# Kernel optimization log

Measured on AMD Instinct MI355X. Metric: run time of the kernel, lower is better.

## Reference

```python
import jax, jax.numpy as jnp
import numpy as np

D_MODEL = 1024
NHEAD = 16
HEAD_DIM = D_MODEL // NHEAD


def setup_inputs() -> dict:
    key = jax.random.key(0)
    ks = jax.random.split(key, 11)
    B, S = 4, 2048
    s = 1.0 / np.sqrt(D_MODEL)
    return {
        "q": jax.random.normal(ks[0], (B, S, D_MODEL), jnp.float32),
        "k": jax.random.normal(ks[1], (B, S, D_MODEL), jnp.float32),
        "v": jax.random.normal(ks[2], (B, S, D_MODEL), jnp.float32),
        "Wq": jax.random.normal(ks[3], (D_MODEL, D_MODEL), jnp.float32) * s,
        "bq": jnp.zeros((D_MODEL,), jnp.float32),
        "Wk": jax.random.normal(ks[4], (D_MODEL, D_MODEL), jnp.float32) * s,
        "bk": jnp.zeros((D_MODEL,), jnp.float32),
        "Wv": jax.random.normal(ks[5], (D_MODEL, D_MODEL), jnp.float32) * s,
        "bv": jnp.zeros((D_MODEL,), jnp.float32),
        "Wo": jax.random.normal(ks[6], (D_MODEL, D_MODEL), jnp.float32) * s,
        "bo": jnp.zeros((D_MODEL,), jnp.float32),
    }


def reference(q, k, v, Wq, bq, Wk, bk, Wv, bv, Wo, bo):
    B, S, _ = q.shape
    H, Dh = NHEAD, HEAD_DIM

    def proj(x, W, b):  # nn.Linear: x @ W.T + b, then split heads -> [B,H,S,Dh]
        y = x @ W.T + b
        return y.reshape(B, S, H, Dh).transpose(0, 2, 1, 3)

    qh = proj(q, Wq, bq)
    kh = proj(k, Wk, bk)
    vh = proj(v, Wv, bv)

    scores = jnp.einsum("bhsd,bhtd->bhst", qh, kh) / jnp.sqrt(jnp.float32(Dh))
    attn = jax.nn.softmax(scores, axis=-1)
    out = jnp.einsum("bhst,bhtd->bhsd", attn, vh)  # [B,H,S,Dh]
    out = out.transpose(0, 2, 1, 3).reshape(B, S, H * Dh)
    return out @ Wo.T + bo
```

## Files before the change

kernel.cpp:

```cpp
#include <hip/hip_runtime.h>


typedef short bf16x8 __attribute__((ext_vector_type(8)));
typedef short bf16x4 __attribute__((ext_vector_type(4)));
typedef float f32x4 __attribute__((ext_vector_type(4)));

__device__ __forceinline__ short f2bf(float x) {
    union { float f; unsigned int u; } un; un.f = x;
    unsigned int u = un.u;
    return (short)(unsigned short)((u + 0x7fffu + ((u >> 16) & 1u)) >> 16);
}

__global__ __launch_bounds__(256) void cvt_bf16(const float* __restrict__ s,
                                                unsigned short* __restrict__ d, int n4) {
    int i = blockIdx.x * blockDim.x + threadIdx.x;
    int stride = gridDim.x * blockDim.x;
    const float4* s4 = reinterpret_cast<const float4*>(s);
    bf16x4* d4 = reinterpret_cast<bf16x4*>(d);
    for (; i < n4; i += stride) {
        float4 x = s4[i];
        bf16x4 y;
        y[0] = f2bf(x.x); y[1] = f2bf(x.y); y[2] = f2bf(x.z); y[3] = f2bf(x.w);
        d4[i] = y;
    }
}

__device__ __forceinline__ void gll16(const void* g, void* l) {
    __builtin_amdgcn_global_load_lds(
        (const __attribute__((address_space(1))) void*)g,
        (__attribute__((address_space(3))) void*)l, 16, 0, 0);
}

template <int MODE>
__global__ __launch_bounds__(256) void gemm_bt(const unsigned short* __restrict__ A,
                                               const unsigned short* __restrict__ Bw,
                                               const float* __restrict__ bias,
                                               float scale,
                                               void* __restrict__ Cout) {
    __shared__ unsigned short As[128 * 32];
    __shared__ unsigned short Bs[128 * 32];
    const int tid = threadIdx.x;
    const int m0 = blockIdx.y * 128, n0 = blockIdx.x * 128;
    const int wave = tid >> 6, lane = tid & 63;
    const int wm = (wave >> 1) * 64, wn = (wave & 1) * 64;
    const int l15 = lane & 15, quad = lane >> 4;
    const int sr = tid >> 2;
    const int sc = (tid & 3) * 8;

    f32x4 acc[4][4] = {};

    for (int k0 = 0; k0 < 1024; k0 += 32) {
        __syncthreads();
#pragma unroll
        for (int ro = 0; ro < 2; ++ro) {
            gll16(&A[(size_t)(m0 + ro * 64 + sr) * 1024 + k0 + sc], &As[ro * 2048 + tid * 8]);
            gll16(&Bw[(size_t)(n0 + ro * 64 + sr) * 1024 + k0 + sc], &Bs[ro * 2048 + tid * 8]);
        }
        __syncthreads();
        bf16x8 a[4], b[4];
#pragma unroll
        for (int i = 0; i < 4; ++i)
            a[i] = *reinterpret_cast<bf16x8*>(&As[(wm + i * 16 + l15) * 32 + quad * 8]);
#pragma unroll
        for (int j = 0; j < 4; ++j)
            b[j] = *reinterpret_cast<bf16x8*>(&Bs[(wn + j * 16 + l15) * 32 + quad * 8]);
#pragma unroll
        for (int i = 0; i < 4; ++i)
#pragma unroll
            for (int j = 0; j < 4; ++j)
                acc[i][j] = __builtin_amdgcn_mfma_f32_16x16x32_bf16(a[i], b[j], acc[i][j], 0, 0, 0);
    }

#pragma unroll
    for (int i = 0; i < 4; ++i) {
#pragma unroll
        for (int j = 0; j < 4; ++j) {
#pragma unroll
            for (int r = 0; r < 4; ++r) {
                int m = m0 + wm + i * 16 + quad * 4 + r;
                int n = n0 + wn + j * 16 + l15;
                float val = (acc[i][j][r] + bias[n]) * scale;
                if (MODE == 0) {
                    reinterpret_cast<float*>(Cout)[(size_t)m * 1024 + n] = val;
                } else {
                    int b_ = m >> 11, s = m & 2047, h = n >> 6, d = n & 63;
                    size_t off = (MODE == 1)
                                     ? ((size_t)((b_ * 16 + h) * 2048 + s) * 64 + d)
                                     : ((size_t)((b_ * 16 + h) * 64 + d) * 2048 + s);
                    reinterpret_cast<unsigned short*>(Cout)[off] = (unsigned short)f2bf(val);
                }
            }
        }
    }
}

__global__ __launch_bounds__(256) void flash_attn(const unsigned short* __restrict__ Qh,
                                                  const unsigned short* __restrict__ Kh,
                                                  const unsigned short* __restrict__ Vt,
                                                  unsigned short* __restrict__ Oa) {
    constexpr int LD = 72;
    __shared__ unsigned short Ks[64 * LD];
    __shared__ unsigned short Vs[64 * LD];
    __shared__ unsigned short Ps[128 * LD];
    const int tid = threadIdx.x;
    const int bh = blockIdx.y;
    const int q0 = blockIdx.x * 128;
    const unsigned short* Qb = Qh + (size_t)bh * 2048 * 64;
    const unsigned short* Kb = Kh + (size_t)bh * 2048 * 64;
    const unsigned short* Vb = Vt + (size_t)bh * 64 * 2048;
    const int wave = tid >> 6, lane = tid & 63;
    const int l15 = lane & 15, quad = lane >> 4;
    const int wq = wave * 32;

    bf16x8 qreg[2][2];
#pragma unroll
    for (int i = 0; i < 2; ++i)
#pragma unroll
        for (int kk = 0; kk < 2; ++kk)
            qreg[i][kk] = *reinterpret_cast<const bf16x8*>(
                &Qb[(size_t)(q0 + wq + i * 16 + l15) * 64 + kk * 32 + quad * 8]);

    f32x4 o[2][4] = {};
    float lpart[2] = {0.f, 0.f};
    const int sr = tid >> 3;
    const int sc = (tid & 7) * 8;

    for (int kv0 = 0; kv0 < 2048; kv0 += 64) {
        __syncthreads();
#pragma unroll
        for (int ro = 0; ro < 2; ++ro) {
            int r = ro * 32 + sr;
            *reinterpret_cast<bf16x8*>(&Ks[r * LD + sc]) =
                *reinterpret_cast<const bf16x8*>(&Kb[(size_t)(kv0 + r) * 64 + sc]);
            *reinterpret_cast<bf16x8*>(&Vs[r * LD + sc]) =
                *reinterpret_cast<const bf16x8*>(&Vb[(size_t)r * 2048 + kv0 + sc]);
        }
        __syncthreads();

        f32x4 sacc[2][4] = {};
#pragma unroll
        for (int kk = 0; kk < 2; ++kk) {
            bf16x8 ak[4];
#pragma unroll
            for (int j = 0; j < 4; ++j)
                ak[j] = *reinterpret_cast<bf16x8*>(&Ks[(j * 16 + l15) * LD + kk * 32 + quad * 8]);
#pragma unroll
            for (int i = 0; i < 2; ++i)
#pragma unroll
                for (int j = 0; j < 4; ++j)
                    sacc[i][j] = __builtin_amdgcn_mfma_f32_16x16x32_bf16(ak[j], qreg[i][kk], sacc[i][j], 0, 0, 0);
        }

#pragma unroll
        for (int i = 0; i < 2; ++i) {
#pragma unroll
            for (int j = 0; j < 4; ++j) {
                float p0 = __expf(sacc[i][j][0]);
                float p1 = __expf(sacc[i][j][1]);
                float p2 = __expf(sacc[i][j][2]);
                float p3 = __expf(sacc[i][j][3]);
                lpart[i] += (p0 + p1) + (p2 + p3);
                bf16x4 pk;
                pk[0] = f2bf(p0); pk[1] = f2bf(p1); pk[2] = f2bf(p2); pk[3] = f2bf(p3);
                *reinterpret_cast<bf16x4*>(&Ps[(wq + i * 16 + l15) * LD + j * 16 + quad * 4]) = pk;
            }
        }

#pragma unroll
        for (int kk = 0; kk < 2; ++kk) {
            bf16x8 ap[2];
#pragma unroll
            for (int i = 0; i < 2; ++i)
                ap[i] = *reinterpret_cast<bf16x8*>(&Ps[(wq + i * 16 + l15) * LD + kk * 32 + quad * 8]);
#pragma unroll
            for (int n = 0; n < 4; ++n) {
                bf16x8 bv = *reinterpret_cast<bf16x8*>(&Vs[(n * 16 + l15) * LD + kk * 32 + quad * 8]);
#pragma unroll
                for (int i = 0; i < 2; ++i)
                    o[i][n] = __builtin_amdgcn_mfma_f32_16x16x32_bf16(ap[i], bv, o[i][n], 0, 0, 0);
            }
        }
    }

    float lt[2];
#pragma unroll
    for (int i = 0; i < 2; ++i) {
        float v = lpart[i];
        v += __shfl_xor(v, 16, 64);
        v += __shfl_xor(v, 32, 64);
        lt[i] = v;
    }
    float rinv[2][4];
#pragma unroll
    for (int i = 0; i < 2; ++i)
#pragma unroll
        for (int r = 0; r < 4; ++r)
            rinv[i][r] = 1.0f / __shfl(lt[i], quad * 4 + r, 64);

    const int b_ = bh >> 4, h = bh & 15;
#pragma unroll
    for (int i = 0; i < 2; ++i)
#pragma unroll
        for (int n = 0; n < 4; ++n)
#pragma unroll
            for (int r = 0; r < 4; ++r) {
                int s = q0 + wq + i * 16 + quad * 4 + r;
                int d = n * 16 + l15;
                Oa[(size_t)(b_ * 2048 + s) * 1024 + h * 64 + d] =
                    (unsigned short)f2bf(o[i][n][r] * rinv[i][r]);
            }
}

extern "C" void kernel_launch(void* const* d_in, const int* in_sizes, int n_in,
                              void* d_out, int out_size, void* d_ws, size_t ws_size,
                              hipStream_t stream) {
    const float* q  = (const float*)d_in[0];
    const float* k  = (const float*)d_in[1];
    const float* v  = (const float*)d_in[2];
    const float* Wq = (const float*)d_in[3];
    const float* bq = (const float*)d_in[4];
    const float* Wk = (const float*)d_in[5];
    const float* bk = (const float*)d_in[6];
    const float* Wv = (const float*)d_in[7];
    const float* bv = (const float*)d_in[8];
    const float* Wo = (const float*)d_in[9];
    const float* bo = (const float*)d_in[10];

    const size_t E = (size_t)8192 * 1024;
    const size_t WE = (size_t)1024 * 1024;
    unsigned short* r0 = (unsigned short*)d_ws;
    unsigned short* r1 = r0 + E;
    unsigned short* r2 = r1 + E;
    unsigned short* r3 = r2 + E;
    unsigned short* wqb = r3 + E;
    unsigned short* wkb = wqb + WE;
    unsigned short* wvb = wkb + WE;
    unsigned short* wob = wvb + WE;

    cvt_bf16<<<2048, 256, 0, stream>>>(q, r0, (int)(E / 4));
    cvt_bf16<<<2048, 256, 0, stream>>>(k, r1, (int)(E / 4));
    cvt_bf16<<<2048, 256, 0, stream>>>(v, r2, (int)(E / 4));
    cvt_bf16<<<1024, 256, 0, stream>>>(Wq, wqb, (int)(WE / 4));
    cvt_bf16<<<1024, 256, 0, stream>>>(Wk, wkb, (int)(WE / 4));
    cvt_bf16<<<1024, 256, 0, stream>>>(Wv, wvb, (int)(WE / 4));
    cvt_bf16<<<1024, 256, 0, stream>>>(Wo, wob, (int)(WE / 4));

    dim3 g(8, 64), blk(256);
    gemm_bt<1><<<g, blk, 0, stream>>>(r0, wqb, bq, 0.125f, r3);
    gemm_bt<1><<<g, blk, 0, stream>>>(r1, wkb, bk, 1.0f, r0);
    gemm_bt<2><<<g, blk, 0, stream>>>(r2, wvb, bv, 1.0f, r1);
    flash_attn<<<dim3(16, 64), blk, 0, stream>>>(r3, r0, r1, r2);
    gemm_bt<0><<<g, blk, 0, stream>>>(r2, wob, bo, 1.0f, (float*)d_out);
}
```

Before: 402.3 us.

## Widen GEMM K-tile, swizzle LDS, async-load attention tiles, batch conversions

The GEMM now stages a K-tile of 64 instead of 32, using XOR-swizzled LDS columns so bank conflicts stay low with the unpadded layout. Flash attention loads K/V tiles with direct global-to-LDS loads into swizzled, unpadded buffers. The softmax uses exp2 with log2(e) folded into the Q scale and packs bf16 with a byte-permute instead of full round-to-nearest-even. The seven conversion launches are merged into two multi-tensor launches. The GEMM mode becomes a runtime argument instead of a template parameter, which adds a branch in the epilogue.

```diff
diff --git a/kernel.cpp b/kernel.cpp
--- a/kernel.cpp
+++ b/kernel.cpp
@@ -11,13 +11,21 @@
     return (short)(unsigned short)((u + 0x7fffu + ((u >> 16) & 1u)) >> 16);
 }
 
-__global__ __launch_bounds__(256) void cvt_bf16(const float* __restrict__ s,
-                                                unsigned short* __restrict__ d, int n4) {
+__device__ __forceinline__ void gll16(const void* g, void* l) {
+    __builtin_amdgcn_global_load_lds(
+        (const __attribute__((address_space(1))) void*)g,
+        (__attribute__((address_space(3))) void*)l, 16, 0, 0);
+}
+
+struct CvtArgs { const float* s[4]; unsigned short* d[4]; int n4; };
+__global__ __launch_bounds__(256) void cvt_bf16(CvtArgs ca) {
+    const float* s = ca.s[blockIdx.y];
+    unsigned short* d = ca.d[blockIdx.y];
     int i = blockIdx.x * blockDim.x + threadIdx.x;
     int stride = gridDim.x * blockDim.x;
     const float4* s4 = reinterpret_cast<const float4*>(s);
     bf16x4* d4 = reinterpret_cast<bf16x4*>(d);
-    for (; i < n4; i += stride) {
+    for (; i < ca.n4; i += stride) {
         float4 x = s4[i];
         bf16x4 y;
         y[0] = f2bf(x.x); y[1] = f2bf(x.y); y[2] = f2bf(x.z); y[3] = f2bf(x.w);
@@ -25,50 +33,48 @@
     }
 }
 
-__device__ __forceinline__ void gll16(const void* g, void* l) {
-    __builtin_amdgcn_global_load_lds(
-        (const __attribute__((address_space(1))) void*)g,
-        (__attribute__((address_space(3))) void*)l, 16, 0, 0);
-}
-
-template <int MODE>
 __global__ __launch_bounds__(256) void gemm_bt(const unsigned short* __restrict__ A,
-                                               const unsigned short* __restrict__ Bw,
+                                               const unsigned short* __restrict__ W,
                                                const float* __restrict__ bias,
-                                               float scale,
-                                               void* __restrict__ Cout) {
-    __shared__ unsigned short As[128 * 32];
-    __shared__ unsigned short Bs[128 * 32];
+                                               float scale, void* __restrict__ out,
+                                               int mode) {
+    __shared__ unsigned short As[128 * 64];
+    __shared__ unsigned short Bs[128 * 64];
     const int tid = threadIdx.x;
     const int m0 = blockIdx.y * 128, n0 = blockIdx.x * 128;
     const int wave = tid >> 6, lane = tid & 63;
     const int wm = (wave >> 1) * 64, wn = (wave & 1) * 64;
     const int l15 = lane & 15, quad = lane >> 4;
-    const int sr = tid >> 2;
-    const int sc = (tid & 3) * 8;
+    const int srow = tid >> 3;
+    const int scol = ((tid & 7) ^ (srow & 7)) * 8;
+    const int cb = (l15 & 7);
 
     f32x4 acc[4][4] = {};
 
-    for (int k0 = 0; k0 < 1024; k0 += 32) {
-        __syncthreads();
-#pragma unroll
-        for (int ro = 0; ro < 2; ++ro) {
-            gll16(&A[(size_t)(m0 + ro * 64 + sr) * 1024 + k0 + sc], &As[ro * 2048 + tid * 8]);
-            gll16(&Bw[(size_t)(n0 + ro * 64 + sr) * 1024 + k0 + sc], &Bs[ro * 2048 + tid * 8]);
-        }
-        __syncthreads();
-        bf16x8 a[4], b[4];
-#pragma unroll
-        for (int i = 0; i < 4; ++i)
-            a[i] = *reinterpret_cast<bf16x8*>(&As[(wm + i * 16 + l15) * 32 + quad * 8]);
-#pragma unroll
-        for (int j = 0; j < 4; ++j)
-            b[j] = *reinterpret_cast<bf16x8*>(&Bs[(wn + j * 16 + l15) * 32 + quad * 8]);
-#pragma unroll
-        for (int i = 0; i < 4; ++i)
+    for (int k0 = 0; k0 < 1024; k0 += 64) {
+        __syncthreads();
+#pragma unroll
+        for (int ro = 0; ro < 4; ++ro) {
+            gll16(&A[(size_t)(m0 + ro * 32 + srow) * 1024 + k0 + scol], &As[ro * 2048 + tid * 8]);
+            gll16(&W[(size_t)(n0 + ro * 32 + srow) * 1024 + k0 + scol], &Bs[ro * 2048 + tid * 8]);
+        }
+        __syncthreads();
+#pragma unroll
+        for (int kk = 0; kk < 2; ++kk) {
+            const int co = ((4 * kk + quad) ^ cb) * 8;
+            bf16x8 a[4], b[4];
+#pragma unroll
+            for (int i = 0; i < 4; ++i)
+                a[i] = *reinterpret_cast<bf16x8*>(&As[(wm + i * 16 + l15) * 64 + co]);
 #pragma unroll
             for (int j = 0; j < 4; ++j)
-                acc[i][j] = __builtin_amdgcn_mfma_f32_16x16x32_bf16(a[i], b[j], acc[i][j], 0, 0, 0);
+                b[j] = *reinterpret_cast<bf16x8*>(&Bs[(wn + j * 16 + l15) * 64 + co]);
+#pragma unroll
+            for (int i = 0; i < 4; ++i)
+#pragma unroll
+                for (int j = 0; j < 4; ++j)
+                    acc[i][j] = __builtin_amdgcn_mfma_f32_16x16x32_bf16(a[i], b[j], acc[i][j], 0, 0, 0);
+        }
     }
 
 #pragma unroll
@@ -80,14 +86,14 @@
                 int m = m0 + wm + i * 16 + quad * 4 + r;
                 int n = n0 + wn + j * 16 + l15;
                 float val = (acc[i][j][r] + bias[n]) * scale;
-                if (MODE == 0) {
-                    reinterpret_cast<float*>(Cout)[(size_t)m * 1024 + n] = val;
+                if (mode == 0) {
+                    reinterpret_cast<float*>(out)[(size_t)m * 1024 + n] = val;
                 } else {
                     int b_ = m >> 11, s = m & 2047, h = n >> 6, d = n & 63;
-                    size_t off = (MODE == 1)
+                    size_t off = (mode == 1)
                                      ? ((size_t)((b_ * 16 + h) * 2048 + s) * 64 + d)
                                      : ((size_t)((b_ * 16 + h) * 64 + d) * 2048 + s);
-                    reinterpret_cast<unsigned short*>(Cout)[off] = (unsigned short)f2bf(val);
+                    reinterpret_cast<unsigned short*>(out)[off] = (unsigned short)f2bf(val);
                 }
             }
         }
@@ -98,10 +104,9 @@
                                                   const unsigned short* __restrict__ Kh,
                                                   const unsigned short* __restrict__ Vt,
                                                   unsigned short* __restrict__ Oa) {
-    constexpr int LD = 72;
-    __shared__ unsigned short Ks[64 * LD];
-    __shared__ unsigned short Vs[64 * LD];
-    __shared__ unsigned short Ps[128 * LD];
+    __shared__ unsigned short Ks[64 * 64];
+    __shared__ unsigned short Vs[64 * 64];
+    __shared__ unsigned short Ps[128 * 72];
     const int tid = threadIdx.x;
     const int bh = blockIdx.y;
     const int q0 = blockIdx.x * 128;
@@ -111,6 +116,9 @@
     const int wave = tid >> 6, lane = tid & 63;
     const int l15 = lane & 15, quad = lane >> 4;
     const int wq = wave * 32;
+    const int srow = tid >> 3;
+    const int scol = ((tid & 7) ^ (srow & 7)) * 8;
+    const int cb = (l15 & 7);
 
     bf16x8 qreg[2][2];
 #pragma unroll
@@ -122,28 +130,24 @@
 
     f32x4 o[2][4] = {};
     float lpart[2] = {0.f, 0.f};
-    const int sr = tid >> 3;
-    const int sc = (tid & 7) * 8;
 
     for (int kv0 = 0; kv0 < 2048; kv0 += 64) {
         __syncthreads();
 #pragma unroll
         for (int ro = 0; ro < 2; ++ro) {
-            int r = ro * 32 + sr;
-            *reinterpret_cast<bf16x8*>(&Ks[r * LD + sc]) =
-                *reinterpret_cast<const bf16x8*>(&Kb[(size_t)(kv0 + r) * 64 + sc]);
-            *reinterpret_cast<bf16x8*>(&Vs[r * LD + sc]) =
-                *reinterpret_cast<const bf16x8*>(&Vb[(size_t)r * 2048 + kv0 + sc]);
+            gll16(&Kb[(size_t)(kv0 + ro * 32 + srow) * 64 + scol], &Ks[ro * 2048 + tid * 8]);
+            gll16(&Vb[(size_t)(ro * 32 + srow) * 2048 + kv0 + scol], &Vs[ro * 2048 + tid * 8]);
         }
         __syncthreads();
 
         f32x4 sacc[2][4] = {};
 #pragma unroll
         for (int kk = 0; kk < 2; ++kk) {
+            const int co = ((4 * kk + quad) ^ cb) * 8;
             bf16x8 ak[4];
 #pragma unroll
             for (int j = 0; j < 4; ++j)
-                ak[j] = *reinterpret_cast<bf16x8*>(&Ks[(j * 16 + l15) * LD + kk * 32 + quad * 8]);
+                ak[j] = *reinterpret_cast<bf16x8*>(&Ks[(j * 16 + l15) * 64 + co]);
 #pragma unroll
             for (int i = 0; i < 2; ++i)
 #pragma unroll
@@ -155,26 +159,29 @@
         for (int i = 0; i < 2; ++i) {
 #pragma unroll
             for (int j = 0; j < 4; ++j) {
-                float p0 = __expf(sacc[i][j][0]);
-                float p1 = __expf(sacc[i][j][1]);
-                float p2 = __expf(sacc[i][j][2]);
-                float p3 = __expf(sacc[i][j][3]);
+                float p0 = __builtin_amdgcn_exp2f(sacc[i][j][0]);
+                float p1 = __builtin_amdgcn_exp2f(sacc[i][j][1]);
+                float p2 = __builtin_amdgcn_exp2f(sacc[i][j][2]);
+                float p3 = __builtin_amdgcn_exp2f(sacc[i][j][3]);
                 lpart[i] += (p0 + p1) + (p2 + p3);
-                bf16x4 pk;
-                pk[0] = f2bf(p0); pk[1] = f2bf(p1); pk[2] = f2bf(p2); pk[3] = f2bf(p3);
-                *reinterpret_cast<bf16x4*>(&Ps[(wq + i * 16 + l15) * LD + j * 16 + quad * 4]) = pk;
+                union { float f; unsigned u; } a0{p0}, a1{p1}, a2{p2}, a3{p3};
+                unsigned lo = __builtin_amdgcn_perm(a1.u + 0x8000u, a0.u + 0x8000u, 0x07060302u);
+                unsigned hi = __builtin_amdgcn_perm(a3.u + 0x8000u, a2.u + 0x8000u, 0x07060302u);
+                uint2 pk; pk.x = lo; pk.y = hi;
+                *reinterpret_cast<uint2*>(&Ps[(wq + i * 16 + l15) * 72 + j * 16 + quad * 4]) = pk;
             }
         }
 
 #pragma unroll
         for (int kk = 0; kk < 2; ++kk) {
+            const int co = ((4 * kk + quad) ^ cb) * 8;
             bf16x8 ap[2];
 #pragma unroll
             for (int i = 0; i < 2; ++i)
-                ap[i] = *reinterpret_cast<bf16x8*>(&Ps[(wq + i * 16 + l15) * LD + kk * 32 + quad * 8]);
+                ap[i] = *reinterpret_cast<bf16x8*>(&Ps[(wq + i * 16 + l15) * 72 + kk * 32 + quad * 8]);
 #pragma unroll
             for (int n = 0; n < 4; ++n) {
-                bf16x8 bv = *reinterpret_cast<bf16x8*>(&Vs[(n * 16 + l15) * LD + kk * 32 + quad * 8]);
+                bf16x8 bv = *reinterpret_cast<bf16x8*>(&Vs[(n * 16 + l15) * 64 + co]);
 #pragma unroll
                 for (int i = 0; i < 2; ++i)
                     o[i][n] = __builtin_amdgcn_mfma_f32_16x16x32_bf16(ap[i], bv, o[i][n], 0, 0, 0);
@@ -237,18 +244,27 @@
     unsigned short* wvb = wkb + WE;
     unsigned short* wob = wvb + WE;
 
-    cvt_bf16<<<2048, 256, 0, stream>>>(q, r0, (int)(E / 4));
-    cvt_bf16<<<2048, 256, 0, stream>>>(k, r1, (int)(E / 4));
-    cvt_bf16<<<2048, 256, 0, stream>>>(v, r2, (int)(E / 4));
-    cvt_bf16<<<1024, 256, 0, stream>>>(Wq, wqb, (int)(WE / 4));
-    cvt_bf16<<<1024, 256, 0, stream>>>(Wk, wkb, (int)(WE / 4));
-    cvt_bf16<<<1024, 256, 0, stream>>>(Wv, wvb, (int)(WE / 4));
-    cvt_bf16<<<1024, 256, 0, stream>>>(Wo, wob, (int)(WE / 4));
-
+    CvtArgs ca;
+    ca.s[0] = q; ca.d[0] = r0;
+    ca.s[1] = k; ca.d[1] = r1;
+    ca.s[2] = v; ca.d[2] = r2;
+    ca.s[3] = q; ca.d[3] = r0;
+    ca.n4 = (int)(E / 4);
+    cvt_bf16<<<dim3(1024, 3), 256, 0, stream>>>(ca);
+
+    CvtArgs cw;
+    cw.s[0] = Wq; cw.d[0] = wqb;
+    cw.s[1] = Wk; cw.d[1] = wkb;
+    cw.s[2] = Wv; cw.d[2] = wvb;
+    cw.s[3] = Wo; cw.d[3] = wob;
+    cw.n4 = (int)(WE / 4);
+    cvt_bf16<<<dim3(256, 4), 256, 0, stream>>>(cw);
+
+    const float QSCALE = 0.125f * 1.44269504088896340736f;
     dim3 g(8, 64), blk(256);
-    gemm_bt<1><<<g, blk, 0, stream>>>(r0, wqb, bq, 0.125f, r3);
-    gemm_bt<1><<<g, blk, 0, stream>>>(r1, wkb, bk, 1.0f, r0);
-    gemm_bt<2><<<g, blk, 0, stream>>>(r2, wvb, bv, 1.0f, r1);
+    gemm_bt<<<g, blk, 0, stream>>>(r0, wqb, bq, QSCALE, r3, 1);
+    gemm_bt<<<g, blk, 0, stream>>>(r1, wkb, bk, 1.0f, r0, 1);
+    gemm_bt<<<g, blk, 0, stream>>>(r2, wvb, bv, 1.0f, r1, 2);
     flash_attn<<<dim3(16, 64), blk, 0, stream>>>(r3, r0, r1, r2);
-    gemm_bt<0><<<g, blk, 0, stream>>>(r2, wob, bo, 1.0f, (float*)d_out);
-}
+    gemm_bt<<<g, blk, 0, stream>>>(r2, wob, bo, 1.0f, d_out, 0);
+}
```

After: 393.0 us. 2.3% less time.
